# Performance work log

Hardware: AMD Instinct MI355X
Metric: run time of the kernel (lower is better)

## Reference

```python
import jax, jax.numpy as jnp
import numpy as np

BATCH_SIZE = 4096
HYPER_LAMBDA = 0.5
EMBED_DIM = 512


def setup_inputs() -> dict:
    key = jax.random.key(0)
    k1, k2 = jax.random.split(key)
    emb_i = jax.random.normal(k1, (BATCH_SIZE, EMBED_DIM), dtype=jnp.float32)
    emb_j = jax.random.normal(k2, (BATCH_SIZE, EMBED_DIM), dtype=jnp.float32)
    return {"emb_i": emb_i, "emb_j": emb_j}


def reference(emb_i, emb_j):
    n = emb_i.shape[0]  # batch_size
    lam = jnp.asarray(HYPER_LAMBDA, dtype=emb_i.dtype)
    # L2-normalize rows (F.normalize, dim=1)
    z_i = emb_i / jnp.linalg.norm(emb_i, axis=1, keepdims=True)
    z_j = emb_j / jnp.linalg.norm(emb_j, axis=1, keepdims=True)
    reps = jnp.concatenate([z_i, z_j], axis=0)  # [2N, D]
    # cosine similarity of already-normalized rows == dot product
    sim = reps @ reps.T  # [2N, 2N]
    # diagonals at offsets +N and -N: sim[k, k+N] and sim[k+N, k]
    idx = jnp.arange(n)
    sim_ij = sim[idx, idx + n]
    sim_ji = sim[idx + n, idx]
    positives = jnp.concatenate([sim_ij, sim_ji], axis=0)  # [2N]
    positives_similarity = jnp.log1p(jnp.exp(-positives + lam))
    neg_mask = 1.0 - jnp.eye(2 * n, dtype=sim.dtype)
    negatives_exp = neg_mask * jnp.exp(sim - lam)
    negatives_similarity = jnp.log1p(negatives_exp)
    positives_sum = jnp.sum(positives_similarity) / (2 * n)
    negatives_sum = jnp.sum(negatives_similarity) / (12 * n)
    return positives_sum + negatives_sum
```

## Files before the change

kernel.cpp:

```cpp
#include <hip/hip_runtime.h>
#include <hip/hip_bf16.h>
#include <hip/hip_fp8.h>
#include <math.h>

typedef float floatx4 __attribute__((ext_vector_type(4)));
typedef long long i64;
typedef long long i64x2 __attribute__((ext_vector_type(2)));

#define N_ROWS 4096
#define DIM 512
#define LAM 0.5f
#define NT 64
#define NTILES (NT * (NT + 1) / 2)
#define GRID 512

#define GLOBAL_AS(p) ((const __attribute__((address_space(1))) void*)(p))
#define LDS_AS(p) ((__attribute__((address_space(3))) void*)(p))

__device__ __forceinline__ unsigned int pack4_fp8(float a, float b, float c, float d) {
    unsigned int u0 = __hip_cvt_float_to_fp8(a, __HIP_SATFINITE, __HIP_E4M3);
    unsigned int u1 = __hip_cvt_float_to_fp8(b, __HIP_SATFINITE, __HIP_E4M3);
    unsigned int u2 = __hip_cvt_float_to_fp8(c, __HIP_SATFINITE, __HIP_E4M3);
    unsigned int u3 = __hip_cvt_float_to_fp8(d, __HIP_SATFINITE, __HIP_E4M3);
    return u0 | (u1 << 8) | (u2 << 16) | (u3 << 24);
}

__global__ __launch_bounds__(256) void normalize_kernel(
    const float* __restrict__ ei, const float* __restrict__ ej,
    unsigned char* __restrict__ Z, float* __restrict__ out) {
    if (blockIdx.x == 0 && threadIdx.x == 0) out[0] = 0.0f;
    const int w = threadIdx.x >> 6, lane = threadIdx.x & 63;
    const int row = blockIdx.x * 4 + w;
    const float* __restrict__ src = (row < N_ROWS)
        ? (ei + (size_t)row * DIM)
        : (ej + (size_t)(row - N_ROWS) * DIM);
    const float4* src4 = (const float4*)src;
    float4 v0 = src4[lane];
    float4 v1 = src4[lane + 64];
    float s = v0.x*v0.x + v0.y*v0.y + v0.z*v0.z + v0.w*v0.w
            + v1.x*v1.x + v1.y*v1.y + v1.z*v1.z + v1.w*v1.w;
    #pragma unroll
    for (int off = 32; off; off >>= 1) s += __shfl_xor(s, off);
    const float r = rsqrtf(s);

    __shared__ __align__(16) unsigned char buf[4][512];
    ((unsigned int*)buf[w])[lane]      = pack4_fp8(v0.x*r, v0.y*r, v0.z*r, v0.w*r);
    ((unsigned int*)buf[w])[lane + 64] = pack4_fp8(v1.x*r, v1.y*r, v1.z*r, v1.w*r);
    __syncthreads();

    const int kt = lane >> 3, q = (lane >> 1) & 3, h = lane & 1;
    i64 val = *(const i64*)(buf[w] + kt * 64 + h * 32 + q * 8);
    const int p = (kt * 4 + q) ^ (row & 7);
    *(i64*)(Z + (size_t)row * DIM + p * 16 + h * 8) = val;
}

__global__ __launch_bounds__(256, 2) void simloss_kernel(
    const unsigned char* __restrict__ Z, float* __restrict__ out) {
    const int tid = threadIdx.x;
    const int w = tid >> 6, lane = tid & 63;
    const int q = lane >> 4, m16 = lane & 15;
    const int wm = w & 1, wn = w >> 1;

    __shared__ __align__(16) unsigned char As[2][128 * 128];
    __shared__ __align__(16) unsigned char Bs[2][128 * 128];
    __shared__ float red[4];

    const int ldsOff = w * 1024;
    const int fragSwz = m16 & 7;
    const int stRow = w * 8 + (lane >> 3);
    const int stCol = (lane & 7) * 16;

    const int bid = blockIdx.x;
    const int nMine = 4 + ((bid & 15) == 0);

    auto decode = [](int id, int& bm, int& bn) {
        int m = (int)((2*NT + 1 - sqrtf((float)((2*NT+1)*(2*NT+1)) - 8.0f * (float)id)) * 0.5f);
        if (m < 0) m = 0; if (m > NT-1) m = NT-1;
        while ((m + 1) * NT - ((m + 1) * m) / 2 <= id) ++m;
        while (m * NT - (m * (m - 1)) / 2 > id) --m;
        bm = m;
        bn = m + (id - (m * NT - (m * (m - 1)) / 2));
    };
    auto tileIdx = [bid](int mt) {
        return (mt < 4) ? (bid + mt * GRID) : (4 * GRID + (bid >> 4));
    };

    int bm, bn; decode(tileIdx(0), bm, bn);
    const unsigned char* stA = Z + (size_t)(bm * 128 + stRow) * DIM + stCol;
    const unsigned char* stB = Z + (size_t)(bn * 128 + stRow) * DIM + stCol;

    float negsum = 0.0f, possum = 0.0f;

    #define ISSUE(par, pA, pB, kOff)                                             \
        _Pragma("unroll")                                                        \
        for (int l = 0; l < 4; ++l) {                                            \
            __builtin_amdgcn_global_load_lds(GLOBAL_AS((pA) + (size_t)l * 32 * DIM + (kOff)), \
                                             LDS_AS(&As[par][ldsOff + l * 4096]), 16, 0, 0);  \
            __builtin_amdgcn_global_load_lds(GLOBAL_AS((pB) + (size_t)l * 32 * DIM + (kOff)), \
                                             LDS_AS(&Bs[par][ldsOff + l * 4096]), 16, 0, 0);  \
        }

    ISSUE(0, stA, stB, 0)

    for (int mt = 0; mt < nMine; ++mt) {
        const int tm = bm * 2 + wm, tn = bn * 2 + wn;
        const bool hasNext = (mt + 1 < nMine);
        int nbm = 0, nbn = 0;
        const unsigned char *nA = stA, *nB = stB;
        if (hasNext) {
            decode(tileIdx(mt + 1), nbm, nbn);
            nA = Z + (size_t)(nbm * 128 + stRow) * DIM + stCol;
            nB = Z + (size_t)(nbn * 128 + stRow) * DIM + stCol;
        }

        floatx4 acc[4][4] = {};

        #pragma unroll
        for (int s = 0; s < 4; ++s) {
            const int par = (mt * 4 + s) & 1;
            asm volatile("s_waitcnt vmcnt(0)" ::: "memory");
            __builtin_amdgcn_sched_barrier(0);
            __builtin_amdgcn_s_barrier();
            if (s < 3)        { ISSUE(par ^ 1, stA, stB, (s + 1) * 128) }
            else if (hasNext) { ISSUE(par ^ 1, nA, nB, 0) }

            const unsigned char* fraA = &As[par][(wm * 64 + m16) * 128];
            const unsigned char* fraB = &Bs[par][(wn * 64 + m16) * 128];
            #pragma unroll
            for (int g = 0; g < 2; ++g) {
                const int cOff = ((g * 4 + q) ^ fragSwz) << 4;
                i64x2 af[4], bf[4];
                #pragma unroll
                for (int i = 0; i < 4; ++i) af[i] = *(const i64x2*)(fraA + i * 16 * 128 + cOff);
                #pragma unroll
                for (int j = 0; j < 4; ++j) bf[j] = *(const i64x2*)(fraB + j * 16 * 128 + cOff);
                __builtin_amdgcn_s_setprio(1);
                #pragma unroll
                for (int i = 0; i < 4; ++i)
                    #pragma unroll
                    for (int j = 0; j < 4; ++j)
                        acc[i][j] = __builtin_amdgcn_mfma_f32_16x16x32_fp8_fp8(af[i].x, bf[j].x, acc[i][j], 0, 0, 0);
                #pragma unroll
                for (int i = 0; i < 4; ++i)
                    #pragma unroll
                    for (int j = 0; j < 4; ++j)
                        acc[i][j] = __builtin_amdgcn_mfma_f32_16x16x32_fp8_fp8(af[i].y, bf[j].y, acc[i][j], 0, 0, 0);
                __builtin_amdgcn_s_setprio(0);
            }
        }

        const float wgt = (tn < tm) ? 0.0f : ((tm == tn) ? 1.0f : 2.0f);
        const bool hasPos = (tn == tm + 64);
        if (wgt != 0.0f) {
            const int rowBase = tm * 64 + q * 4;
            const int colBase = tn * 64 + m16;
            float nacc = 0.0f;
            #pragma unroll
            for (int j = 0; j < 4; ++j) {
                const int cg = colBase + j * 16;
                float p = 1.0f;
                #pragma unroll
                for (int i = 0; i < 4; ++i) {
                    const int rg0 = rowBase + i * 16;
                    #pragma unroll
                    for (int r = 0; r < 4; ++r) {
                        const float sv = acc[i][j][r];
                        float e = __expf(sv - LAM);
                        if (rg0 + r == cg) e = 0.0f;
                        p *= (1.0f + e);
                        if (hasPos && cg == rg0 + r + N_ROWS)
                            possum += log1pf(expf(-sv + LAM));
                    }
                }
                nacc += __logf(p);
            }
            negsum += nacc * wgt;
        }

        bm = nbm; bn = nbn; stA = nA; stB = nB;
    }

    #pragma unroll
    for (int off = 32; off; off >>= 1) {
        negsum += __shfl_xor(negsum, off);
        possum += __shfl_xor(possum, off);
    }
    const float part = negsum * (1.0f / (12.0f * (float)N_ROWS))
                     + possum * (1.0f / (float)N_ROWS);
    if (lane == 0) red[w] = part;
    __syncthreads();
    if (tid == 0) atomicAdd(out, red[0] + red[1] + red[2] + red[3]);
    #undef ISSUE
}

extern "C" void kernel_launch(void* const* d_in, const int* in_sizes, int n_in,
                              void* d_out, int out_size, void* d_ws, size_t ws_size,
                              hipStream_t stream) {
    const float* ei = (const float*)d_in[0];
    const float* ej = (const float*)d_in[1];
    float* out = (float*)d_out;
    unsigned char* Z = (unsigned char*)d_ws;

    normalize_kernel<<<2048, 256, 0, stream>>>(ei, ej, Z, out);
    simloss_kernel<<<GRID, 256, 0, stream>>>(Z, out);
}
```

Measured before the change: 101.3 us.

## Enlarge simloss block tile to 256x256 with eight waves

Doubles the block tile edge from 128 to 256 and uses 512 threads (8 waves, each computing a 64x128 subtile), halving the number of blocks and triangular tiles. The goal is better operand reuse per LDS/global load and less diagonal-tile waste. In exchange, LDS usage rises to 128KB per block and accumulator register use doubles, which likely limits occupancy to one block per CU and reduces latency hiding; setprio hints are also removed.

```diff
diff --git a/kernel.cpp b/kernel.cpp
--- a/kernel.cpp
+++ b/kernel.cpp
@@ -10,9 +10,9 @@
 #define N_ROWS 4096
 #define DIM 512
 #define LAM 0.5f
-#define NT 64
-#define NTILES (NT * (NT + 1) / 2)
-#define GRID 512
+#define NT2 32
+#define NTILES2 (NT2 * (NT2 + 1) / 2)
+#define GRID 256
 
 #define GLOBAL_AS(p) ((const __attribute__((address_space(1))) void*)(p))
 #define LDS_AS(p) ((__attribute__((address_space(3))) void*)(p))
@@ -54,16 +54,16 @@
     *(i64*)(Z + (size_t)row * DIM + p * 16 + h * 8) = val;
 }
 
-__global__ __launch_bounds__(256, 2) void simloss_kernel(
+__global__ __launch_bounds__(512, 2) void simloss_kernel(
     const unsigned char* __restrict__ Z, float* __restrict__ out) {
     const int tid = threadIdx.x;
     const int w = tid >> 6, lane = tid & 63;
     const int q = lane >> 4, m16 = lane & 15;
-    const int wm = w & 1, wn = w >> 1;
-
-    __shared__ __align__(16) unsigned char As[2][128 * 128];
-    __shared__ __align__(16) unsigned char Bs[2][128 * 128];
-    __shared__ float red[4];
+    const int wr = w & 3, wc = w >> 2;
+
+    __shared__ __align__(16) unsigned char As[2][256 * 128];
+    __shared__ __align__(16) unsigned char Bs[2][256 * 128];
+    __shared__ float red[8];
 
     const int ldsOff = w * 1024;
     const int fragSwz = m16 & 7;
@@ -71,49 +71,48 @@
     const int stCol = (lane & 7) * 16;
 
     const int bid = blockIdx.x;
-    const int nMine = 4 + ((bid & 15) == 0);
+    const int nMine = 2 + ((bid & 15) == 0);
 
     auto decode = [](int id, int& bm, int& bn) {
-        int m = (int)((2*NT + 1 - sqrtf((float)((2*NT+1)*(2*NT+1)) - 8.0f * (float)id)) * 0.5f);
-        if (m < 0) m = 0; if (m > NT-1) m = NT-1;
-        while ((m + 1) * NT - ((m + 1) * m) / 2 <= id) ++m;
-        while (m * NT - (m * (m - 1)) / 2 > id) --m;
+        int m = (int)((2*NT2 + 1 - sqrtf((float)((2*NT2+1)*(2*NT2+1)) - 8.0f * (float)id)) * 0.5f);
+        if (m < 0) m = 0; if (m > NT2-1) m = NT2-1;
+        while ((m + 1) * NT2 - ((m + 1) * m) / 2 <= id) ++m;
+        while (m * NT2 - (m * (m - 1)) / 2 > id) --m;
         bm = m;
-        bn = m + (id - (m * NT - (m * (m - 1)) / 2));
+        bn = m + (id - (m * NT2 - (m * (m - 1)) / 2));
     };
     auto tileIdx = [bid](int mt) {
-        return (mt < 4) ? (bid + mt * GRID) : (4 * GRID + (bid >> 4));
+        return (mt < 2) ? (bid + mt * GRID) : (2 * GRID + (bid >> 4));
     };
 
     int bm, bn; decode(tileIdx(0), bm, bn);
-    const unsigned char* stA = Z + (size_t)(bm * 128 + stRow) * DIM + stCol;
-    const unsigned char* stB = Z + (size_t)(bn * 128 + stRow) * DIM + stCol;
+    const unsigned char* stA = Z + (size_t)(bm * 256 + stRow) * DIM + stCol;
+    const unsigned char* stB = Z + (size_t)(bn * 256 + stRow) * DIM + stCol;
 
     float negsum = 0.0f, possum = 0.0f;
 
     #define ISSUE(par, pA, pB, kOff)                                             \
         _Pragma("unroll")                                                        \
         for (int l = 0; l < 4; ++l) {                                            \
-            __builtin_amdgcn_global_load_lds(GLOBAL_AS((pA) + (size_t)l * 32 * DIM + (kOff)), \
-                                             LDS_AS(&As[par][ldsOff + l * 4096]), 16, 0, 0);  \
-            __builtin_amdgcn_global_load_lds(GLOBAL_AS((pB) + (size_t)l * 32 * DIM + (kOff)), \
-                                             LDS_AS(&Bs[par][ldsOff + l * 4096]), 16, 0, 0);  \
+            __builtin_amdgcn_global_load_lds(GLOBAL_AS((pA) + (size_t)l * 64 * DIM + (kOff)), \
+                                             LDS_AS(&As[par][l * 8192 + ldsOff]), 16, 0, 0);  \
+            __builtin_amdgcn_global_load_lds(GLOBAL_AS((pB) + (size_t)l * 64 * DIM + (kOff)), \
+                                             LDS_AS(&Bs[par][l * 8192 + ldsOff]), 16, 0, 0);  \
         }
 
     ISSUE(0, stA, stB, 0)
 
     for (int mt = 0; mt < nMine; ++mt) {
-        const int tm = bm * 2 + wm, tn = bn * 2 + wn;
         const bool hasNext = (mt + 1 < nMine);
         int nbm = 0, nbn = 0;
         const unsigned char *nA = stA, *nB = stB;
         if (hasNext) {
             decode(tileIdx(mt + 1), nbm, nbn);
-            nA = Z + (size_t)(nbm * 128 + stRow) * DIM + stCol;
-            nB = Z + (size_t)(nbn * 128 + stRow) * DIM + stCol;
-        }
-
-        floatx4 acc[4][4] = {};
+            nA = Z + (size_t)(nbm * 256 + stRow) * DIM + stCol;
+            nB = Z + (size_t)(nbn * 256 + stRow) * DIM + stCol;
+        }
+
+        floatx4 acc[4][8] = {};
 
         #pragma unroll
         for (int s = 0; s < 4; ++s) {
@@ -124,57 +123,54 @@
             if (s < 3)        { ISSUE(par ^ 1, stA, stB, (s + 1) * 128) }
             else if (hasNext) { ISSUE(par ^ 1, nA, nB, 0) }
 
-            const unsigned char* fraA = &As[par][(wm * 64 + m16) * 128];
-            const unsigned char* fraB = &Bs[par][(wn * 64 + m16) * 128];
+            const unsigned char* fraA = &As[par][(wr * 64 + m16) * 128];
+            const unsigned char* fraB = &Bs[par][(wc * 128 + m16) * 128];
             #pragma unroll
             for (int g = 0; g < 2; ++g) {
                 const int cOff = ((g * 4 + q) ^ fragSwz) << 4;
-                i64x2 af[4], bf[4];
+                i64x2 af[4], bf[8];
                 #pragma unroll
                 for (int i = 0; i < 4; ++i) af[i] = *(const i64x2*)(fraA + i * 16 * 128 + cOff);
                 #pragma unroll
-                for (int j = 0; j < 4; ++j) bf[j] = *(const i64x2*)(fraB + j * 16 * 128 + cOff);
-                __builtin_amdgcn_s_setprio(1);
+                for (int j = 0; j < 8; ++j) bf[j] = *(const i64x2*)(fraB + j * 16 * 128 + cOff);
                 #pragma unroll
                 for (int i = 0; i < 4; ++i)
                     #pragma unroll
-                    for (int j = 0; j < 4; ++j)
+                    for (int j = 0; j < 8; ++j)
                         acc[i][j] = __builtin_amdgcn_mfma_f32_16x16x32_fp8_fp8(af[i].x, bf[j].x, acc[i][j], 0, 0, 0);
                 #pragma unroll
                 for (int i = 0; i < 4; ++i)
                     #pragma unroll
-                    for (int j = 0; j < 4; ++j)
+                    for (int j = 0; j < 8; ++j)
                         acc[i][j] = __builtin_amdgcn_mfma_f32_16x16x32_fp8_fp8(af[i].y, bf[j].y, acc[i][j], 0, 0, 0);
-                __builtin_amdgcn_s_setprio(0);
             }
         }
 
-        const float wgt = (tn < tm) ? 0.0f : ((tm == tn) ? 1.0f : 2.0f);
-        const bool hasPos = (tn == tm + 64);
-        if (wgt != 0.0f) {
-            const int rowBase = tm * 64 + q * 4;
-            const int colBase = tn * 64 + m16;
-            float nacc = 0.0f;
+        const int tm = bm * 4 + wr;
+        const int rowBase = bm * 256 + wr * 64 + q * 4;
+        const int colBase = bn * 256 + wc * 128 + m16;
+        #pragma unroll
+        for (int j = 0; j < 8; ++j) {
+            const int tn = bn * 4 + wc * 2 + (j >> 2);
+            const float wgt = (tn < tm) ? 0.0f : ((tn == tm) ? 1.0f : 2.0f);
+            const bool hasPos = (tn == tm + 64);
+            if (wgt == 0.0f) continue;
+            const int cg = colBase + j * 16;
+            float p = 1.0f;
             #pragma unroll
-            for (int j = 0; j < 4; ++j) {
-                const int cg = colBase + j * 16;
-                float p = 1.0f;
-                #pragma unroll
-                for (int i = 0; i < 4; ++i) {
-                    const int rg0 = rowBase + i * 16;
-                    #pragma unroll
-                    for (int r = 0; r < 4; ++r) {
-                        const float sv = acc[i][j][r];
-                        float e = __expf(sv - LAM);
-                        if (rg0 + r == cg) e = 0.0f;
-                        p *= (1.0f + e);
-                        if (hasPos && cg == rg0 + r + N_ROWS)
-                            possum += log1pf(expf(-sv + LAM));
-                    }
+            for (int i = 0; i < 4; ++i) {
+                const int rg0 = rowBase + i * 16;
+                #pragma unroll
+                for (int r = 0; r < 4; ++r) {
+                    const float sv = acc[i][j][r];
+                    float e = __expf(sv - LAM);
+                    if (rg0 + r == cg) e = 0.0f;
+                    p *= (1.0f + e);
+                    if (hasPos && cg == rg0 + r + N_ROWS)
+                        possum += log1pf(expf(-sv + LAM));
                 }
-                nacc += __logf(p);
             }
-            negsum += nacc * wgt;
+            negsum += __logf(p) * wgt;
         }
 
         bm = nbm; bn = nbn; stA = nA; stB = nB;
@@ -189,7 +185,12 @@
                      + possum * (1.0f / (float)N_ROWS);
     if (lane == 0) red[w] = part;
     __syncthreads();
-    if (tid == 0) atomicAdd(out, red[0] + red[1] + red[2] + red[3]);
+    if (tid == 0) {
+        float t = 0.0f;
+        #pragma unroll
+        for (int i = 0; i < 8; ++i) t += red[i];
+        atomicAdd(out, t);
+    }
     #undef ISSUE
 }
 
@@ -202,5 +203,5 @@
     unsigned char* Z = (unsigned char*)d_ws;
 
     normalize_kernel<<<2048, 256, 0, stream>>>(ei, ej, Z, out);
-    simloss_kernel<<<GRID, 256, 0, stream>>>(Z, out);
-}
+    simloss_kernel<<<GRID, 512, 0, stream>>>(Z, out);
+}
```

New measurement: 119.2 us. +17.6%, slower.

## Switch GEMM to 32x32x64 scaled FP8 MFMA with matching fragment layout

Applied to the files above, without the earlier changes.

Replaces the 16x16x32 FP8 MFMA tiling (4x4 accumulators, 32 instructions per k-step group) with the gfx950 32x32x64 f8f6f4 scaled MFMA using a 2x2 grid of 16-element accumulators. The global Z swizzle written by the normalize kernel and the LDS fragment addressing are changed to match the new operand layout, and the epilogue index mapping is rewritten for the 32x32 output layout. The aim is to cut MFMA issue count and LDS fragment reads per tile. The risk is in the correctness of the scale arguments and the swizzle mapping, and in a different register footprint.

```diff
diff --git a/kernel.cpp b/kernel.cpp
--- a/kernel.cpp
+++ b/kernel.cpp
@@ -4,8 +4,10 @@
 #include <math.h>
 
 typedef float floatx4 __attribute__((ext_vector_type(4)));
+typedef float floatx16 __attribute__((ext_vector_type(16)));
+typedef int i32x4 __attribute__((ext_vector_type(4)));
+typedef int i32x8 __attribute__((ext_vector_type(8)));
 typedef long long i64;
-typedef long long i64x2 __attribute__((ext_vector_type(2)));
 
 #define N_ROWS 4096
 #define DIM 512
@@ -48,27 +50,27 @@
     ((unsigned int*)buf[w])[lane + 64] = pack4_fp8(v1.x*r, v1.y*r, v1.z*r, v1.w*r);
     __syncthreads();
 
-    const int kt = lane >> 3, q = (lane >> 1) & 3, h = lane & 1;
-    i64 val = *(const i64*)(buf[w] + kt * 64 + h * 32 + q * 8);
-    const int p = (kt * 4 + q) ^ (row & 7);
-    *(i64*)(Z + (size_t)row * DIM + p * 16 + h * 8) = val;
+    const int ch = lane >> 1, h2 = lane & 1;
+    i64 val = *(const i64*)(buf[w] + ch * 16 + h2 * 8);
+    const int p = ch ^ (row & 7);
+    *(i64*)(Z + (size_t)row * DIM + p * 16 + h2 * 8) = val;
 }
 
 __global__ __launch_bounds__(256, 2) void simloss_kernel(
     const unsigned char* __restrict__ Z, float* __restrict__ out) {
     const int tid = threadIdx.x;
     const int w = tid >> 6, lane = tid & 63;
-    const int q = lane >> 4, m16 = lane & 15;
+    const int r5 = lane & 31, h = lane >> 5;
+    const int rx = r5 & 7;
     const int wm = w & 1, wn = w >> 1;
 
     __shared__ __align__(16) unsigned char As[2][128 * 128];
     __shared__ __align__(16) unsigned char Bs[2][128 * 128];
     __shared__ float red[4];
 
-    const int ldsOff = w * 1024;
-    const int fragSwz = m16 & 7;
     const int stRow = w * 8 + (lane >> 3);
     const int stCol = (lane & 7) * 16;
+    const int ldsOff = w * 1024;
 
     const int bid = blockIdx.x;
     const int nMine = 4 + ((bid & 15) == 0);
@@ -95,15 +97,14 @@
         _Pragma("unroll")                                                        \
         for (int l = 0; l < 4; ++l) {                                            \
             __builtin_amdgcn_global_load_lds(GLOBAL_AS((pA) + (size_t)l * 32 * DIM + (kOff)), \
-                                             LDS_AS(&As[par][ldsOff + l * 4096]), 16, 0, 0);  \
+                                             LDS_AS(&As[par][ldsOff + l * 4096]), 16, 0, 0); \
             __builtin_amdgcn_global_load_lds(GLOBAL_AS((pB) + (size_t)l * 32 * DIM + (kOff)), \
-                                             LDS_AS(&Bs[par][ldsOff + l * 4096]), 16, 0, 0);  \
+                                             LDS_AS(&Bs[par][ldsOff + l * 4096]), 16, 0, 0); \
         }
 
     ISSUE(0, stA, stB, 0)
 
     for (int mt = 0; mt < nMine; ++mt) {
-        const int tm = bm * 2 + wm, tn = bn * 2 + wn;
         const bool hasNext = (mt + 1 < nMine);
         int nbm = 0, nbn = 0;
         const unsigned char *nA = stA, *nB = stB;
@@ -113,7 +114,7 @@
             nB = Z + (size_t)(nbn * 128 + stRow) * DIM + stCol;
         }
 
-        floatx4 acc[4][4] = {};
+        floatx16 acc[2][2] = {};
 
         #pragma unroll
         for (int s = 0; s < 4; ++s) {
@@ -124,51 +125,51 @@
             if (s < 3)        { ISSUE(par ^ 1, stA, stB, (s + 1) * 128) }
             else if (hasNext) { ISSUE(par ^ 1, nA, nB, 0) }
 
-            const unsigned char* fraA = &As[par][(wm * 64 + m16) * 128];
-            const unsigned char* fraB = &Bs[par][(wn * 64 + m16) * 128];
+            const unsigned char* fraA = &As[par][(wm * 64 + r5) * 128];
+            const unsigned char* fraB = &Bs[par][(wn * 64 + r5) * 128];
             #pragma unroll
-            for (int g = 0; g < 2; ++g) {
-                const int cOff = ((g * 4 + q) ^ fragSwz) << 4;
-                i64x2 af[4], bf[4];
-                #pragma unroll
-                for (int i = 0; i < 4; ++i) af[i] = *(const i64x2*)(fraA + i * 16 * 128 + cOff);
-                #pragma unroll
-                for (int j = 0; j < 4; ++j) bf[j] = *(const i64x2*)(fraB + j * 16 * 128 + cOff);
-                __builtin_amdgcn_s_setprio(1);
-                #pragma unroll
-                for (int i = 0; i < 4; ++i)
-                    #pragma unroll
-                    for (int j = 0; j < 4; ++j)
-                        acc[i][j] = __builtin_amdgcn_mfma_f32_16x16x32_fp8_fp8(af[i].x, bf[j].x, acc[i][j], 0, 0, 0);
-                #pragma unroll
-                for (int i = 0; i < 4; ++i)
-                    #pragma unroll
-                    for (int j = 0; j < 4; ++j)
-                        acc[i][j] = __builtin_amdgcn_mfma_f32_16x16x32_fp8_fp8(af[i].y, bf[j].y, acc[i][j], 0, 0, 0);
-                __builtin_amdgcn_s_setprio(0);
+            for (int g2 = 0; g2 < 2; ++g2) {
+                const int o0 = ((g2 * 4 + h * 2) ^ rx) << 4;
+                const int o1 = o0 ^ 16;
+                i32x4 al0 = *(const i32x4*)(fraA + o0);
+                i32x4 al1 = *(const i32x4*)(fraA + o1);
+                i32x4 am0 = *(const i32x4*)(fraA + 32 * 128 + o0);
+                i32x4 am1 = *(const i32x4*)(fraA + 32 * 128 + o1);
+                i32x4 bl0 = *(const i32x4*)(fraB + o0);
+                i32x4 bl1 = *(const i32x4*)(fraB + o1);
+                i32x4 bm0 = *(const i32x4*)(fraB + 32 * 128 + o0);
+                i32x4 bm1 = *(const i32x4*)(fraB + 32 * 128 + o1);
+                i32x8 a0 = __builtin_shufflevector(al0, al1, 0,1,2,3,4,5,6,7);
+                i32x8 a1 = __builtin_shufflevector(am0, am1, 0,1,2,3,4,5,6,7);
+                i32x8 b0 = __builtin_shufflevector(bl0, bl1, 0,1,2,3,4,5,6,7);
+                i32x8 b1 = __builtin_shufflevector(bm0, bm1, 0,1,2,3,4,5,6,7);
+                acc[0][0] = __builtin_amdgcn_mfma_scale_f32_32x32x64_f8f6f4(a0, b0, acc[0][0], 0, 0, 0, 127, 0, 127);
+                acc[0][1] = __builtin_amdgcn_mfma_scale_f32_32x32x64_f8f6f4(a0, b1, acc[0][1], 0, 0, 0, 127, 0, 127);
+                acc[1][0] = __builtin_amdgcn_mfma_scale_f32_32x32x64_f8f6f4(a1, b0, acc[1][0], 0, 0, 0, 127, 0, 127);
+                acc[1][1] = __builtin_amdgcn_mfma_scale_f32_32x32x64_f8f6f4(a1, b1, acc[1][1], 0, 0, 0, 127, 0, 127);
             }
         }
 
-        const float wgt = (tn < tm) ? 0.0f : ((tm == tn) ? 1.0f : 2.0f);
+        const int tm = bm * 2 + wm, tn = bn * 2 + wn;
+        const float wgt = (tn < tm) ? 0.0f : ((tn == tm) ? 1.0f : 2.0f);
         const bool hasPos = (tn == tm + 64);
         if (wgt != 0.0f) {
-            const int rowBase = tm * 64 + q * 4;
-            const int colBase = tn * 64 + m16;
             float nacc = 0.0f;
             #pragma unroll
-            for (int j = 0; j < 4; ++j) {
-                const int cg = colBase + j * 16;
+            for (int j = 0; j < 2; ++j) {
+                const int cg = tn * 64 + j * 32 + r5;
                 float p = 1.0f;
                 #pragma unroll
-                for (int i = 0; i < 4; ++i) {
-                    const int rg0 = rowBase + i * 16;
+                for (int i = 0; i < 2; ++i) {
+                    const int rbase = tm * 64 + i * 32 + 4 * h;
                     #pragma unroll
-                    for (int r = 0; r < 4; ++r) {
-                        const float sv = acc[i][j][r];
+                    for (int reg = 0; reg < 16; ++reg) {
+                        const int rg = rbase + (reg & 3) + 8 * (reg >> 2);
+                        const float sv = acc[i][j][reg];
                         float e = __expf(sv - LAM);
-                        if (rg0 + r == cg) e = 0.0f;
+                        if (rg == cg) e = 0.0f;
                         p *= (1.0f + e);
-                        if (hasPos && cg == rg0 + r + N_ROWS)
+                        if (hasPos && cg == rg + N_ROWS)
                             possum += log1pf(expf(-sv + LAM));
                     }
                 }
```

Result: slower. 151.7 us (+49.7%).

## Switch to triple-buffered 64-wide K stages with partial vmcnt waits

Applied to the files above, without the earlier changes.

The GEMM pipeline changes from double-buffered 128-wide K slices to triple-buffered 64-wide slices, prefetching two stages ahead. It waits with vmcnt(4) instead of draining every load, so global-to-LDS copies can overlap more with MFMA work. The fp8 swizzle in the normalize kernel and the fragment reads are shrunk from 8 to 4 chunks to match the narrower rows. The cost is twice as many barriers per tile and possibly more LDS bank conflicts from the weaker swizzle.

```diff
diff --git a/kernel.cpp b/kernel.cpp
--- a/kernel.cpp
+++ b/kernel.cpp
@@ -50,7 +50,7 @@
 
     const int kt = lane >> 3, q = (lane >> 1) & 3, h = lane & 1;
     i64 val = *(const i64*)(buf[w] + kt * 64 + h * 32 + q * 8);
-    const int p = (kt * 4 + q) ^ (row & 7);
+    const int p = (kt * 4 + q) ^ (row & 3);
     *(i64*)(Z + (size_t)row * DIM + p * 16 + h * 8) = val;
 }
 
@@ -61,14 +61,14 @@
     const int q = lane >> 4, m16 = lane & 15;
     const int wm = w & 1, wn = w >> 1;
 
-    __shared__ __align__(16) unsigned char As[2][128 * 128];
-    __shared__ __align__(16) unsigned char Bs[2][128 * 128];
+    __shared__ __align__(16) unsigned char As[3][128 * 64];
+    __shared__ __align__(16) unsigned char Bs[3][128 * 64];
     __shared__ float red[4];
 
-    const int ldsOff = w * 1024;
-    const int fragSwz = m16 & 7;
-    const int stRow = w * 8 + (lane >> 3);
-    const int stCol = (lane & 7) * 16;
+    const int fragSwz = m16 & 3;
+    const int stRow = w * 32 + (lane >> 2);
+    const int stCol = (lane & 3) * 16;
+    const int ldsOff = w * 2048;
 
     const int bid = blockIdx.x;
     const int nMine = 4 + ((bid & 15) == 0);
@@ -91,19 +91,19 @@
 
     float negsum = 0.0f, possum = 0.0f;
 
-    #define ISSUE(par, pA, pB, kOff)                                             \
+    #define ISSUE(b, pA, pB, kOff)                                               \
         _Pragma("unroll")                                                        \
-        for (int l = 0; l < 4; ++l) {                                            \
-            __builtin_amdgcn_global_load_lds(GLOBAL_AS((pA) + (size_t)l * 32 * DIM + (kOff)), \
-                                             LDS_AS(&As[par][ldsOff + l * 4096]), 16, 0, 0);  \
-            __builtin_amdgcn_global_load_lds(GLOBAL_AS((pB) + (size_t)l * 32 * DIM + (kOff)), \
-                                             LDS_AS(&Bs[par][ldsOff + l * 4096]), 16, 0, 0);  \
+        for (int l = 0; l < 2; ++l) {                                            \
+            __builtin_amdgcn_global_load_lds(GLOBAL_AS((pA) + (size_t)l * 16 * DIM + (kOff)), \
+                                             LDS_AS(&As[b][ldsOff + l * 1024]), 16, 0, 0); \
+            __builtin_amdgcn_global_load_lds(GLOBAL_AS((pB) + (size_t)l * 16 * DIM + (kOff)), \
+                                             LDS_AS(&Bs[b][ldsOff + l * 1024]), 16, 0, 0); \
         }
 
     ISSUE(0, stA, stB, 0)
+    ISSUE(1, stA, stB, 64)
 
     for (int mt = 0; mt < nMine; ++mt) {
-        const int tm = bm * 2 + wm, tn = bn * 2 + wn;
         const bool hasNext = (mt + 1 < nMine);
         int nbm = 0, nbn = 0;
         const unsigned char *nA = stA, *nB = stB;
@@ -116,40 +116,40 @@
         floatx4 acc[4][4] = {};
 
         #pragma unroll
-        for (int s = 0; s < 4; ++s) {
-            const int par = (mt * 4 + s) & 1;
-            asm volatile("s_waitcnt vmcnt(0)" ::: "memory");
+        for (int u = 0; u < 8; ++u) {
+            const int g = mt * 8 + u;
+            const int b = g % 3;
+            if (u == 7 && !hasNext) { asm volatile("s_waitcnt vmcnt(0)" ::: "memory"); }
+            else                    { asm volatile("s_waitcnt vmcnt(4)" ::: "memory"); }
             __builtin_amdgcn_sched_barrier(0);
             __builtin_amdgcn_s_barrier();
-            if (s < 3)        { ISSUE(par ^ 1, stA, stB, (s + 1) * 128) }
-            else if (hasNext) { ISSUE(par ^ 1, nA, nB, 0) }
-
-            const unsigned char* fraA = &As[par][(wm * 64 + m16) * 128];
-            const unsigned char* fraB = &Bs[par][(wn * 64 + m16) * 128];
-            #pragma unroll
-            for (int g = 0; g < 2; ++g) {
-                const int cOff = ((g * 4 + q) ^ fragSwz) << 4;
-                i64x2 af[4], bf[4];
+            if (u < 6)         { ISSUE((g + 2) % 3, stA, stB, (u + 2) * 64) }
+            else if (hasNext)  { ISSUE((g + 2) % 3, nA, nB, (u - 6) * 64) }
+
+            const unsigned char* fraA = &As[b][(wm * 64 + m16) * 64];
+            const unsigned char* fraB = &Bs[b][(wn * 64 + m16) * 64];
+            const int cOff = (q ^ fragSwz) << 4;
+            i64x2 af[4], bf[4];
+            #pragma unroll
+            for (int i = 0; i < 4; ++i) af[i] = *(const i64x2*)(fraA + i * 16 * 64 + cOff);
+            #pragma unroll
+            for (int j = 0; j < 4; ++j) bf[j] = *(const i64x2*)(fraB + j * 16 * 64 + cOff);
+            __builtin_amdgcn_s_setprio(1);
+            #pragma unroll
+            for (int i = 0; i < 4; ++i)
                 #pragma unroll
-                for (int i = 0; i < 4; ++i) af[i] = *(const i64x2*)(fraA + i * 16 * 128 + cOff);
+                for (int j = 0; j < 4; ++j)
+                    acc[i][j] = __builtin_amdgcn_mfma_f32_16x16x32_fp8_fp8(af[i].x, bf[j].x, acc[i][j], 0, 0, 0);
+            #pragma unroll
+            for (int i = 0; i < 4; ++i)
                 #pragma unroll
-                for (int j = 0; j < 4; ++j) bf[j] = *(const i64x2*)(fraB + j * 16 * 128 + cOff);
-                __builtin_amdgcn_s_setprio(1);
-                #pragma unroll
-                for (int i = 0; i < 4; ++i)
-                    #pragma unroll
-                    for (int j = 0; j < 4; ++j)
-                        acc[i][j] = __builtin_amdgcn_mfma_f32_16x16x32_fp8_fp8(af[i].x, bf[j].x, acc[i][j], 0, 0, 0);
-                #pragma unroll
-                for (int i = 0; i < 4; ++i)
-                    #pragma unroll
-                    for (int j = 0; j < 4; ++j)
-                        acc[i][j] = __builtin_amdgcn_mfma_f32_16x16x32_fp8_fp8(af[i].y, bf[j].y, acc[i][j], 0, 0, 0);
-                __builtin_amdgcn_s_setprio(0);
-            }
-        }
-
-        const float wgt = (tn < tm) ? 0.0f : ((tm == tn) ? 1.0f : 2.0f);
+                for (int j = 0; j < 4; ++j)
+                    acc[i][j] = __builtin_amdgcn_mfma_f32_16x16x32_fp8_fp8(af[i].y, bf[j].y, acc[i][j], 0, 0, 0);
+            __builtin_amdgcn_s_setprio(0);
+        }
+
+        const int tm = bm * 2 + wm, tn = bn * 2 + wn;
+        const float wgt = (tn < tm) ? 0.0f : ((tn == tm) ? 1.0f : 2.0f);
         const bool hasPos = (tn == tm + 64);
         if (wgt != 0.0f) {
             const int rowBase = tm * 64 + q * 4;
```

After: 106.4 us. 1.05x slower.
